# Kernel tuning notes

Measured on AMD Instinct MI355X. Metric: run time of the kernel, lower is better.

Reference implementation:

```python
import jax, jax.numpy as jnp
import numpy as np
from jax import lax

NUM_IM, ROIS = 32, 128          # images per batch, proposals per image
NUM_CLASSES, EMBED, OBJ_DIM = 151, 200, 2048
HALF_H = 256                    # per-direction LSTM hidden; bi concat -> 512
BN_EPS = 1e-5


def _lstm_dir(xs, wih, whh, b):
    # xs: [T, B, Din] -> hidden states [T, B, H]
    pre = jnp.einsum('tbd,dh->tbh', xs, wih) + b  # precompute input proj
    H = whh.shape[0]
    h0 = jnp.zeros((xs.shape[1], H), xs.dtype)
    def step(carry, pt):
        h, c = carry
        g = pt + h @ whh
        i, f, gg, o = jnp.split(g, 4, axis=-1)
        c = jax.nn.sigmoid(f) * c + jax.nn.sigmoid(i) * jnp.tanh(gg)
        h = jax.nn.sigmoid(o) * jnp.tanh(c)
        return (h, c), h
    _, hs = lax.scan(step, (h0, h0), pre)
    return hs


def _bilstm(x, wih, whh, b):
    # x: [B, T, D] -> [B, T, 2*HALF_H]; wih/whh/b carry both directions on axis 0
    xs = jnp.swapaxes(x, 0, 1)
    fwd = _lstm_dir(xs, wih[0], whh[0], b[0])
    bwd = _lstm_dir(xs[::-1], wih[1], whh[1], b[1])[::-1]
    return jnp.swapaxes(jnp.concatenate([fwd, bwd], -1), 0, 1)


def _context(feats, conf, params):
    # sort_rois: per-image descending confidence order, run 2-layer bi(tree)LSTM,
    # then scatter back with the inverse permutation (as in _sort_by_score).
    D = feats.shape[-1]
    f = feats.reshape(NUM_IM, ROIS, D)
    perm = jnp.argsort(-conf.reshape(NUM_IM, ROIS), axis=1)
    xs = jnp.take_along_axis(f, perm[..., None], axis=1)
    wih0, whh0, b0, wih1, whh1, b1 = params
    h = _bilstm(xs, wih0, whh0, b0)
    h = _bilstm(h, wih1, whh1, b1)
    inv = jnp.argsort(perm, axis=1)
    h = jnp.take_along_axis(h, inv[..., None], axis=1)
    return h.reshape(NUM_IM * ROIS, -1)


def setup_inputs() -> dict:
    key = jax.random.key(0)
    ks = jax.random.split(key, 24)
    N = NUM_IM * ROIS
    obj_fmaps = jax.random.normal(ks[0], (N, OBJ_DIM), jnp.float32)
    obj_logits = jax.random.normal(ks[1], (N, NUM_CLASSES), jnp.float32)
    xy = jax.random.uniform(ks[2], (N, 2), jnp.float32) * 500.0
    wh = jax.random.uniform(ks[3], (N, 2), jnp.float32) * 100.0 + 1.0
    boxes = jnp.concatenate([xy, xy + wh], axis=1)  # valid x1y1x2y2
    im_inds = jnp.repeat(jnp.arange(NUM_IM, dtype=jnp.int64), ROIS)
    w = lambda k, s: (jax.random.normal(k, s, jnp.float32) * 0.02)
    H4 = 4 * HALF_H
    D_obj, D_edge = OBJ_DIM + EMBED + 128, EMBED + 2 * HALF_H + OBJ_DIM
    return {
        'obj_fmaps': obj_fmaps, 'obj_logits': obj_logits, 'boxes': boxes,
        'im_inds': im_inds,
        'obj_embed_w': w(ks[4], (NUM_CLASSES, EMBED)),
        'obj_embed2_w': w(ks[5], (NUM_CLASSES, EMBED)),
        'bn_gamma': jnp.ones((4,), jnp.float32), 'bn_beta': jnp.zeros((4,), jnp.float32),
        'bn_mean': jnp.zeros((4,), jnp.float32), 'bn_var': jnp.ones((4,), jnp.float32),
        'pos_w': w(ks[6], (4, 128)), 'pos_b': jnp.zeros((128,), jnp.float32),
        'obj_wih0': w(ks[7], (2, D_obj, H4)), 'obj_whh0': w(ks[8], (2, HALF_H, H4)),
        'obj_b0': jnp.zeros((2, H4), jnp.float32),
        'obj_wih1': w(ks[9], (2, 2 * HALF_H, H4)), 'obj_whh1': w(ks[10], (2, HALF_H, H4)),
        'obj_b1': jnp.zeros((2, H4), jnp.float32),
        'edge_wih0': w(ks[11], (2, D_edge, H4)), 'edge_whh0': w(ks[12], (2, HALF_H, H4)),
        'edge_b0': jnp.zeros((2, H4), jnp.float32),
        'edge_wih1': w(ks[13], (2, 2 * HALF_H, H4)), 'edge_whh1': w(ks[14], (2, HALF_H, H4)),
        'edge_b1': jnp.zeros((2, H4), jnp.float32),
        'dec_w': w(ks[15], (D_obj + 2 * HALF_H, NUM_CLASSES)),
        'dec_b': jnp.zeros((NUM_CLASSES,), jnp.float32),
    }


def reference(obj_fmaps, obj_logits, boxes, im_inds, obj_embed_w, obj_embed2_w,
              bn_gamma, bn_beta, bn_mean, bn_var, pos_w, pos_b,
              obj_wih0, obj_whh0, obj_b0, obj_wih1, obj_whh1, obj_b1,
              edge_wih0, edge_whh0, edge_b0, edge_wih1, edge_whh1, edge_b1,
              dec_w, dec_b):
    probs = jax.nn.softmax(obj_logits, axis=-1)
    obj_embed = probs @ obj_embed_w                      # soft class embedding
    x1, y1, x2, y2 = boxes[:, 0], boxes[:, 1], boxes[:, 2], boxes[:, 3]
    cs = jnp.stack([(x1 + x2) * 0.5, (y1 + y2) * 0.5, x2 - x1, y2 - y1], axis=-1)
    csn = (cs - bn_mean) * lax.rsqrt(bn_var + BN_EPS) * bn_gamma + bn_beta
    pos = jax.nn.relu(csn @ pos_w + pos_b)               # BN(4)+Linear(4,128)+ReLU
    feats = jnp.concatenate([obj_fmaps, obj_embed, pos], axis=-1)  # [N, 2376]
    conf = jnp.max(probs[:, 1:], axis=-1)                # confidence (non-bg)
    enc = _context(feats, conf, (obj_wih0, obj_whh0, obj_b0,
                                 obj_wih1, obj_whh1, obj_b1))       # [N, 512]
    dec_in = jnp.concatenate([feats, enc], axis=-1)      # pass_in_obj_feats_to_decoder
    obj_dists = dec_in @ dec_w + dec_b                   # [N, 151]
    obj_preds = jnp.argmax(obj_dists[:, 1:], axis=-1) + 1
    edge_in = jnp.concatenate([obj_embed2_w[obj_preds], enc, obj_fmaps], axis=-1)
    edge_ctx = _context(edge_in, conf, (edge_wih0, edge_whh0, edge_b0,
                                        edge_wih1, edge_whh1, edge_b1))  # [N, 512]
    return jnp.concatenate([obj_dists, edge_ctx], axis=-1)  # [N, 663]
```

## Files before the change

kernel.cpp:

```cpp
#include <hip/hip_runtime.h>
#include <hip/hip_bf16.h>
#include <hip/hip_fp16.h>

typedef unsigned short u16;
typedef unsigned char u8;
typedef unsigned int u32;
typedef short s16x8 __attribute__((ext_vector_type(8)));
typedef float f32x4 __attribute__((ext_vector_type(4)));
typedef int i32x4 __attribute__((ext_vector_type(4)));

#define FE_LD 2944
#define EDGE_LD 2816

static __device__ __forceinline__ int sdot4(u32 a, u32 b, int acc) {
  return __builtin_amdgcn_sdot4((int)a, (int)b, acc, false);
}
static __device__ __forceinline__ float fsig(float x) {
  return __builtin_amdgcn_rcpf(1.f + __expf(-x));
}
static __device__ __forceinline__ float ftanh(float x) {
  return 1.f - 2.f * __builtin_amdgcn_rcpf(1.f + __expf(2.f * x));
}

#define GLD_LDS16(gsrc, ldst) \
  __builtin_amdgcn_global_load_lds((const __attribute__((address_space(1))) void*)(gsrc), \
                                   (__attribute__((address_space(3))) void*)(ldst), 16, 0, 0)

static __device__ __forceinline__ void xcd_map(int gy, int* bx, int* by) {
  int lin = blockIdx.x;
  int q = gridDim.x >> 3;
  int wg = (lin & 7) * q + (lin >> 3);
  *bx = wg / gy; *by = wg % gy;
}

__global__ __launch_bounds__(256) void gemm_kernel(
    const u16* __restrict__ A, int lda,
    const u16* __restrict__ B, int ldb,
    int K, int N, int gy,
    float* __restrict__ outF, __hip_bfloat16* __restrict__ outB, int ldc,
    const float* __restrict__ bias)
{
  __shared__ __align__(16) u16 As[128*64];
  __shared__ __align__(16) u16 Bs[128*64];
  const int tid = threadIdx.x;
  const int w = tid >> 6, lane = tid & 63;
  const int wm = w >> 1, wn = w & 1;
  int bxi, byi; xcd_map(gy, &bxi, &byi);
  const long bm = (long)bxi * 128;
  const long bn = (long)byi * 128;
  f32x4 acc[4][4] = {};

  for (int k0 = 0; k0 < K; k0 += 64) {
    #pragma unroll
    for (int rr = 0; rr < 4; rr++) {
      int idx = rr * 256 + tid;
      int row = idx >> 3;
      int g   = idx & 7;
      int gs  = g ^ (row & 7);
      int ldst = (rr * 256 + (w << 6)) * 8;
      GLD_LDS16(A + (bm + row) * (long)lda + k0 + gs * 8, &As[ldst]);
      GLD_LDS16(B + (bn + row) * (long)ldb + k0 + gs * 8, &Bs[ldst]);
    }
    __syncthreads();
    #pragma unroll
    for (int kk = 0; kk < 2; kk++) {
      s16x8 af[4], bfr[4];
      #pragma unroll
      for (int i = 0; i < 4; i++) {
        int ra = wm * 64 + i * 16 + (lane & 15);
        int rb = wn * 64 + i * 16 + (lane & 15);
        int gg = kk * 4 + (lane >> 4);
        af[i]  = *(const s16x8*)&As[ra * 64 + ((gg ^ (ra & 7)) << 3)];
        bfr[i] = *(const s16x8*)&Bs[rb * 64 + ((gg ^ (rb & 7)) << 3)];
      }
      #pragma unroll
      for (int i = 0; i < 4; i++)
        #pragma unroll
        for (int j = 0; j < 4; j++)
          acc[i][j] = __builtin_amdgcn_mfma_f32_16x16x32_bf16(af[i], bfr[j], acc[i][j], 0, 0, 0);
    }
    __syncthreads();
  }

  #pragma unroll
  for (int i = 0; i < 4; i++)
    #pragma unroll
    for (int j = 0; j < 4; j++)
      #pragma unroll
      for (int v = 0; v < 4; v++) {
        long rr = bm + wm * 64 + i * 16 + (lane >> 4) * 4 + v;
        int  cc = (int)bn + wn * 64 + j * 16 + (lane & 15);
        if (cc < N) {
          float val = acc[i][j][v] + (bias ? bias[cc] : 0.f);
          if (outF) outF[rr * (long)ldc + cc] = val;
          else      outB[rr * (long)ldc + cc] = __float2bfloat16(val);
        }
      }
}

__global__ __launch_bounds__(256) void gemm_i8_kernel(
    const u8* __restrict__ A, int lda,
    const u8* __restrict__ B, int ldb,
    int K, int N, int gy,
    const float* __restrict__ asc, const float* __restrict__ bsc,
    __hip_bfloat16* __restrict__ outB, int ldc,
    const float* __restrict__ bias)
{
  __shared__ __align__(16) u8 As[128*128];
  __shared__ __align__(16) u8 Bs[128*128];
  const int tid = threadIdx.x;
  const int w = tid >> 6, lane = tid & 63;
  const int wm = w >> 1, wn = w & 1;
  int bxi, byi; xcd_map(gy, &bxi, &byi);
  const long bm = (long)bxi * 128;
  const long bn = (long)byi * 128;
  i32x4 acc[4][4] = {};

  for (int k0 = 0; k0 < K; k0 += 128) {
    #pragma unroll
    for (int rr = 0; rr < 4; rr++) {
      int idx = rr * 256 + tid;
      int row = idx >> 3;
      int g   = idx & 7;
      int gs  = g ^ (row & 7);
      int ldst = (rr * 256 + (w << 6)) * 16;
      GLD_LDS16(A + (bm + row) * (long)lda + k0 + gs * 16, &As[ldst]);
      GLD_LDS16(B + (bn + row) * (long)ldb + k0 + gs * 16, &Bs[ldst]);
    }
    __syncthreads();
    #pragma unroll
    for (int kk = 0; kk < 2; kk++) {
      i32x4 af[4], bfr[4];
      #pragma unroll
      for (int i = 0; i < 4; i++) {
        int ra = wm * 64 + i * 16 + (lane & 15);
        int rb = wn * 64 + i * 16 + (lane & 15);
        int gg = kk * 4 + (lane >> 4);
        af[i]  = __builtin_bit_cast(i32x4, *(const uint4*)&As[ra * 128 + ((gg ^ (ra & 7)) << 4)]);
        bfr[i] = __builtin_bit_cast(i32x4, *(const uint4*)&Bs[rb * 128 + ((gg ^ (rb & 7)) << 4)]);
      }
      #pragma unroll
      for (int i = 0; i < 4; i++)
        #pragma unroll
        for (int j = 0; j < 4; j++)
          acc[i][j] = __builtin_amdgcn_mfma_i32_16x16x64_i8(af[i], bfr[j], acc[i][j], 0, 0, 0);
    }
    __syncthreads();
  }

  #pragma unroll
  for (int i = 0; i < 4; i++)
    #pragma unroll
    for (int j = 0; j < 4; j++)
      #pragma unroll
      for (int v = 0; v < 4; v++) {
        long rr = bm + wm * 64 + i * 16 + (lane >> 4) * 4 + v;
        int  cc = (int)bn + wn * 64 + j * 16 + (lane & 15);
        if (cc < N) {
          float val = (float)acc[i][j][v] * asc[rr] * bsc[cc] + (bias ? bias[cc] : 0.f);
          outB[rr * (long)ldc + cc] = __float2bfloat16(val);
        }
      }
}

__global__ void quant_rows(const u16* __restrict__ src, long ld, int K,
                           u8* __restrict__ dst, long dld, float* __restrict__ scale)
{
  __shared__ float red[256];
  const int row = blockIdx.x, t = threadIdx.x;
  const u16* s = src + (size_t)row * ld;
  float mx = 0.f;
  for (int c = t; c < K; c += 256) {
    u32 u = (u32)s[c] << 16;
    mx = fmaxf(mx, fabsf(__builtin_bit_cast(float, u)));
  }
  red[t] = mx; __syncthreads();
  for (int st = 128; st > 0; st >>= 1) { if (t < st) red[t] = fmaxf(red[t], red[t + st]); __syncthreads(); }
  mx = red[0];
  float inv = (mx > 0.f) ? 127.f / mx : 0.f;
  if (t == 0) scale[row] = (mx > 0.f) ? mx / 127.f : 0.f;
  u32* d32 = (u32*)(dst + (size_t)row * dld);
  for (int wd = t; wd < (K >> 2); wd += 256) {
    u32 v = 0;
    #pragma unroll
    for (int b = 0; b < 4; b++) {
      u32 u = (u32)s[4 * wd + b] << 16;
      int q = __float2int_rn(__builtin_bit_cast(float, u) * inv);
      q = max(-127, min(127, q));
      v |= ((u32)(q & 0xff)) << (8 * b);
    }
    d32[wd] = v;
  }
}

#define N_TROPS 10
struct TrOps {
  const float* src[N_TROPS];
  __hip_bfloat16* dst[N_TROPS];
  int srcK[N_TROPS], srcN[N_TROPS], dstR[N_TROPS], dstC[N_TROPS];
  int split[N_TROPS], soff[N_TROPS];
  int tileBase[N_TROPS], tilesX[N_TROPS];
};
__global__ void transpose_batch(TrOps ops)
{
  __shared__ float tile[32][33];
  int bid = blockIdx.x;
  int op = 0;
  #pragma unroll
  for (int i = 1; i < N_TROPS; i++) if (bid >= ops.tileBase[i]) op = i;
  const int local = bid - ops.tileBase[op];
  const int kt = (local % ops.tilesX[op]) * 32;
  const int nt = (local / ops.tilesX[op]) * 32;
  const float* src = ops.src[op];
  __hip_bfloat16* dst = ops.dst[op];
  const int srcK = ops.srcK[op], srcN = ops.srcN[op];
  const int dstR = ops.dstR[op], dstC = ops.dstC[op];
  const int split = ops.split[op], soff = ops.soff[op];

  const int tx = threadIdx.x & 31, ty = threadIdx.x >> 5;
  for (int i = ty; i < 32; i += 8) {
    int k = kt + i;
    int srck = (k < split) ? (soff + k) : (k - split);
    int n = nt + tx;
    tile[i][tx] = (srck < srcK && n < srcN) ? src[(size_t)srck * srcN + n] : 0.f;
  }
  __syncthreads();
  for (int i = ty; i < 32; i += 8) {
    int n = nt + i, k = kt + tx;
    if (n < dstR && k < dstC)
      dst[(size_t)n * dstC + k] = __float2bfloat16(tile[tx][i]);
  }
}

struct PkOps {
  const float* whh[4];
  u32* wreg[4];
  u32* wlds[4];
  float* wsc[4];
};
__global__ void pack_batch(PkOps ops)
{
  const int set = blockIdx.y;
  const float* whh = ops.whh[set];
  u32* wreg = ops.wreg[set];
  u32* wlds = ops.wlds[set];
  float* wsc = ops.wsc[set];

  const int idx = blockIdx.x * 256 + threadIdx.x;
  const int d = idx >> 10, col = idx & 1023;
  const int c4 = col >> 8, j = col & 255;
  const float* s = whh + (size_t)d * 256 * 1024 + col;
  float mx = 0.f;
  for (int k = 0; k < 256; k++) mx = fmaxf(mx, fabsf(s[(size_t)k * 1024]));
  float inv = (mx > 0.f) ? 127.f / mx : 0.f;
  wsc[d * 1024 + col] = (mx > 0.f) ? mx / (127.f * 127.f) : 0.f;
  const int rc = (c4 < 2) ? 12 : 8;
  const int rb = (c4 == 0) ? 0 : (c4 == 1) ? 12 : (c4 == 2) ? 24 : 32;
  for (int kg = 0; kg < 4; kg++) {
    const int slot = kg * 256 + j;
    for (int w = 0; w < 16; w++) {
      u32 v = 0;
      #pragma unroll
      for (int b = 0; b < 4; b++) {
        int q = __float2int_rn(s[(size_t)(kg * 64 + 4 * w + b) * 1024] * inv);
        q = max(-127, min(127, q));
        v |= ((u32)(q & 0xff)) << (8 * b);
      }
      if (w < rc) {
        wreg[(size_t)(d * 40 + rb + w) * 1024 + slot] = v;
      } else {
        int qq, comp;
        if (c4 == 0)      { qq = 0; comp = w - 12; }
        else if (c4 == 1) { qq = 1; comp = w - 12; }
        else if (c4 == 2) { qq = 2 + ((w - 8) >> 2); comp = (w - 8) & 3; }
        else              { qq = 4 + ((w - 8) >> 2); comp = (w - 8) & 3; }
        wlds[((size_t)(d * 6 + qq) * 1024 + slot) * 4 + comp] = v;
      }
    }
  }
}

__global__ void prep_kernel(
    const float* __restrict__ logits, const float* __restrict__ fmaps,
    const float* __restrict__ boxes,
    const float* __restrict__ bn_g, const float* __restrict__ bn_b,
    const float* __restrict__ bn_m, const float* __restrict__ bn_v,
    const float* __restrict__ pos_w, const float* __restrict__ pos_b,
    __hip_bfloat16* __restrict__ FE, __hip_bfloat16* __restrict__ probsb,
    float* __restrict__ conf)
{
  __shared__ float red[256];
  const int row = blockIdx.x, t = threadIdx.x;
  float v = (t < 151) ? logits[(size_t)row * 151 + t] : -3.0e38f;
  red[t] = v; __syncthreads();
  for (int s = 128; s > 0; s >>= 1) { if (t < s) red[t] = fmaxf(red[t], red[t + s]); __syncthreads(); }
  float mx = red[0]; __syncthreads();
  float p = (t < 151) ? expf(v - mx) : 0.f;
  red[t] = p; __syncthreads();
  for (int s = 128; s > 0; s >>= 1) { if (t < s) red[t] += red[t + s]; __syncthreads(); }
  float sum = red[0]; __syncthreads();
  p = p / sum;
  if (t < 192) probsb[(size_t)row * 192 + t] = __float2bfloat16((t < 151) ? p : 0.f);
  red[t] = (t >= 1 && t < 151) ? p : 0.f; __syncthreads();
  for (int s = 128; s > 0; s >>= 1) { if (t < s) red[t] = fmaxf(red[t], red[t + s]); __syncthreads(); }
  if (t == 0) conf[row] = red[0];

  if (t < 128) {
    float x1 = boxes[row * 4 + 0], y1 = boxes[row * 4 + 1];
    float x2 = boxes[row * 4 + 2], y2 = boxes[row * 4 + 3];
    float cs[4] = { (x1 + x2) * 0.5f, (y1 + y2) * 0.5f, x2 - x1, y2 - y1 };
    float a = pos_b[t];
    #pragma unroll
    for (int j = 0; j < 4; j++) {
      float cn = (cs[j] - bn_m[j]) * rsqrtf(bn_v[j] + 1e-5f) * bn_g[j] + bn_b[j];
      a += cn * pos_w[j * 128 + t];
    }
    FE[(size_t)row * FE_LD + 2760 + t] = __float2bfloat16(fmaxf(a, 0.f));
  }
  for (int c0 = t; c0 < 2048; c0 += 256)
    FE[(size_t)row * FE_LD + 512 + c0] = __float2bfloat16(fmaps[(size_t)row * 2048 + c0]);
}

__global__ void sort_kernel(const float* __restrict__ conf, int* __restrict__ perm)
{
  __shared__ float key[128];
  __shared__ int   idx[128];
  const int b = blockIdx.x, t = threadIdx.x;
  key[t] = conf[b * 128 + t]; idx[t] = t;
  __syncthreads();
  for (int k = 2; k <= 128; k <<= 1)
    for (int j = k >> 1; j > 0; j >>= 1) {
      int ixj = t ^ j;
      if (ixj > t) {
        bool up = (t & k) == 0;
        float ka = key[t], kb = key[ixj];
        int ia = idx[t], ib = idx[ixj];
        bool before = (ka > kb) || (ka == kb && ia < ib);
        if (before != up) { key[t] = kb; key[ixj] = ka; idx[t] = ib; idx[ixj] = ia; }
      }
      __syncthreads();
    }
  perm[b * 128 + t] = b * 128 + idx[t];
}

__global__ __launch_bounds__(1024) void rec_kernel(
    const __hip_bfloat16* __restrict__ P,
    const int* __restrict__ perm,
    const u32* __restrict__ wreg_g,
    const uint4* __restrict__ wlds_g,
    const float* __restrict__ wsc_g,
    int gatherPerm, int outPerm,
    __hip_bfloat16* __restrict__ out_bf, int out_ld,
    float* __restrict__ out_f32, int f32_ld, int f32_off)
{
  __shared__ __align__(16) uint4 wt4[6 * 1024];
  __shared__ __align__(16) int4 part[256 * 5];
  __shared__ __align__(16) u32 hq[64];
  __shared__ int prow_lds[128];
  const int tid = threadIdx.x;
  const int kg = tid >> 8;
  const int img = blockIdx.x & 31, dir = blockIdx.x >> 5;

  u32 wv[40];
  {
    const u32* rp = wreg_g + (size_t)dir * 40960 + tid;
    #pragma unroll
    for (int i = 0; i < 40; i++) wv[i] = rp[(size_t)i * 1024];
  }
  #pragma unroll
  for (int i = 0; i < 40; i++) asm volatile("" : "+v"(wv[i]));
  {
    const uint4* lp = wlds_g + (size_t)dir * 6144 + tid;
    #pragma unroll
    for (int q = 0; q < 6; q++) wt4[q * 1024 + tid] = lp[(size_t)q * 1024];
  }
  if (tid < 128) prow_lds[tid] = perm[img * 128 + tid];
  if (tid < 64) hq[tid] = 0;

  float sc0 = 0.f, sc1 = 0.f, sc2 = 0.f, sc3 = 0.f, cst = 0.f;
  if (tid < 256) {
    const float* sp = wsc_g + dir * 1024 + tid;
    sc0 = sp[0]; sc1 = sp[256]; sc2 = sp[512]; sc3 = sp[768];
  }
  __syncthreads();

  const uint4* hq4 = (const uint4*)hq;

  int st = dir ? 127 : 0;
  float p0 = 0.f, p1 = 0.f, p2 = 0.f, p3 = 0.f;
  if (tid < 256) {
    int prow0 = gatherPerm ? prow_lds[st] : (img * 128 + st);
    const __hip_bfloat16* pp = P + (size_t)prow0 * 2048 + dir * 1024 + tid;
    p0 = __bfloat162float(pp[0]);   p1 = __bfloat162float(pp[256]);
    p2 = __bfloat162float(pp[512]); p3 = __bfloat162float(pp[768]);
  }

  for (int t = 0; t < 128; t++) {
    float n0 = 0.f, n1 = 0.f, n2 = 0.f, n3 = 0.f;
    if (tid < 256 && t < 127) {
      int stn = dir ? (126 - t) : (t + 1);
      int prn = gatherPerm ? prow_lds[stn] : (img * 128 + stn);
      const __hip_bfloat16* pp = P + (size_t)prn * 2048 + dir * 1024 + tid;
      n0 = __bfloat162float(pp[0]);   n1 = __bfloat162float(pp[256]);
      n2 = __bfloat162float(pp[512]); n3 = __bfloat162float(pp[768]);
    }

    int a0 = 0, a1 = 0, a2 = 0, a3 = 0;
    {
      uint4 hv = hq4[kg * 4 + 0];
      a0 = sdot4(hv.x, wv[0], a0);  a0 = sdot4(hv.y, wv[1], a0);
      a0 = sdot4(hv.z, wv[2], a0);  a0 = sdot4(hv.w, wv[3], a0);
      a1 = sdot4(hv.x, wv[12], a1); a1 = sdot4(hv.y, wv[13], a1);
      a1 = sdot4(hv.z, wv[14], a1); a1 = sdot4(hv.w, wv[15], a1);
      a2 = sdot4(hv.x, wv[24], a2); a2 = sdot4(hv.y, wv[25], a2);
      a2 = sdot4(hv.z, wv[26], a2); a2 = sdot4(hv.w, wv[27], a2);
      a3 = sdot4(hv.x, wv[32], a3); a3 = sdot4(hv.y, wv[33], a3);
      a3 = sdot4(hv.z, wv[34], a3); a3 = sdot4(hv.w, wv[35], a3);
    }
    {
      uint4 hv = hq4[kg * 4 + 1];
      a0 = sdot4(hv.x, wv[4], a0);  a0 = sdot4(hv.y, wv[5], a0);
      a0 = sdot4(hv.z, wv[6], a0);  a0 = sdot4(hv.w, wv[7], a0);
      a1 = sdot4(hv.x, wv[16], a1); a1 = sdot4(hv.y, wv[17], a1);
      a1 = sdot4(hv.z, wv[18], a1); a1 = sdot4(hv.w, wv[19], a1);
      a2 = sdot4(hv.x, wv[28], a2); a2 = sdot4(hv.y, wv[29], a2);
      a2 = sdot4(hv.z, wv[30], a2); a2 = sdot4(hv.w, wv[31], a2);
      a3 = sdot4(hv.x, wv[36], a3); a3 = sdot4(hv.y, wv[37], a3);
      a3 = sdot4(hv.z, wv[38], a3); a3 = sdot4(hv.w, wv[39], a3);
    }
    {
      uint4 hv = hq4[kg * 4 + 2];
      a0 = sdot4(hv.x, wv[8], a0);  a0 = sdot4(hv.y, wv[9], a0);
      a0 = sdot4(hv.z, wv[10], a0); a0 = sdot4(hv.w, wv[11], a0);
      a1 = sdot4(hv.x, wv[20], a1); a1 = sdot4(hv.y, wv[21], a1);
      a1 = sdot4(hv.z, wv[22], a1); a1 = sdot4(hv.w, wv[23], a1);
      uint4 wl = wt4[2 * 1024 + tid];
      a2 = sdot4(hv.x, wl.x, a2); a2 = sdot4(hv.y, wl.y, a2);
      a2 = sdot4(hv.z, wl.z, a2); a2 = sdot4(hv.w, wl.w, a2);
      wl = wt4[4 * 1024 + tid];
      a3 = sdot4(hv.x, wl.x, a3); a3 = sdot4(hv.y, wl.y, a3);
      a3 = sdot4(hv.z, wl.z, a3); a3 = sdot4(hv.w, wl.w, a3);
    }
    {
      uint4 hv = hq4[kg * 4 + 3];
      uint4 wl = wt4[0 * 1024 + tid];
      a0 = sdot4(hv.x, wl.x, a0); a0 = sdot4(hv.y, wl.y, a0);
      a0 = sdot4(hv.z, wl.z, a0); a0 = sdot4(hv.w, wl.w, a0);
      wl = wt4[1 * 1024 + tid];
      a1 = sdot4(hv.x, wl.x, a1); a1 = sdot4(hv.y, wl.y, a1);
      a1 = sdot4(hv.z, wl.z, a1); a1 = sdot4(hv.w, wl.w, a1);
      wl = wt4[3 * 1024 + tid];
      a2 = sdot4(hv.x, wl.x, a2); a2 = sdot4(hv.y, wl.y, a2);
      a2 = sdot4(hv.z, wl.z, a2); a2 = sdot4(hv.w, wl.w, a2);
      wl = wt4[5 * 1024 + tid];
      a3 = sdot4(hv.x, wl.x, a3); a3 = sdot4(hv.y, wl.y, a3);
      a3 = sdot4(hv.z, wl.z, a3); a3 = sdot4(hv.w, wl.w, a3);
    }

    part[(tid & 255) * 5 + kg] = int4{a0, a1, a2, a3};
    __syncthreads();

    if (tid < 256) {
      int4 q0 = part[tid * 5 + 0], q1 = part[tid * 5 + 1];
      int4 q2 = part[tid * 5 + 2], q3 = part[tid * 5 + 3];
      float gi = (float)(q0.x + q1.x + q2.x + q3.x) * sc0 + p0;
      float gf = (float)(q0.y + q1.y + q2.y + q3.y) * sc1 + p1;
      float gg = (float)(q0.z + q1.z + q2.z + q3.z) * sc2 + p2;
      float go = (float)(q0.w + q1.w + q2.w + q3.w) * sc3 + p3;
      float si = fsig(gi), sf = fsig(gf), so = fsig(go);
      cst = sf * cst + si * ftanh(gg);
      float h = so * ftanh(cst);
      int qi = __float2int_rn(h * 127.f);
      ((signed char*)hq)[tid] = (signed char)qi;
      const int orow = outPerm ? prow_lds[st] : (img * 128 + st);
      if (out_bf)  out_bf[(size_t)orow * out_ld + dir * 256 + tid] = __float2bfloat16(h);
      if (out_f32) out_f32[(size_t)orow * f32_ld + f32_off + dir * 256 + tid] = h;
    }
    __syncthreads();
    p0 = n0; p1 = n1; p2 = n2; p3 = n3;
    st = dir ? (st - 1) : (st + 1);
  }
}

__global__ void argmax_edge_kernel(const float* __restrict__ dists,
                                   const float* __restrict__ embed2,
                                   const float* __restrict__ fmaps,
                                   const __hip_bfloat16* __restrict__ FE,
                                   __hip_bfloat16* __restrict__ EDGE)
{
  __shared__ float rv[256];
  __shared__ int   ri[256];
  const int row = blockIdx.x, t = threadIdx.x;

  float best = (t < 150) ? dists[(size_t)row * 663 + 1 + t] : -3.4e38f;
  int   bi   = (t < 150) ? (1 + t) : 1000;
  rv[t] = best; ri[t] = bi;
  __syncthreads();
  for (int s = 128; s > 0; s >>= 1) {
    if (t < s) {
      float ov = rv[t + s]; int oi = ri[t + s];
      if (ov > rv[t] || (ov == rv[t] && oi < ri[t])) { rv[t] = ov; ri[t] = oi; }
    }
    __syncthreads();
  }
  const int pr = ri[0];

  for (int c0 = t; c0 < 200; c0 += 256)
    EDGE[(size_t)row * EDGE_LD + c0] = __float2bfloat16(embed2[(size_t)pr * 200 + c0]);
  for (int c0 = t; c0 < 512; c0 += 256)
    EDGE[(size_t)row * EDGE_LD + 200 + c0] = FE[(size_t)row * FE_LD + c0];
  for (int c0 = t; c0 < 2048; c0 += 256)
    EDGE[(size_t)row * EDGE_LD + 712 + c0] = __float2bfloat16(fmaps[(size_t)row * 2048 + c0]);
}

extern "C" void kernel_launch(void* const* d_in, const int* in_sizes, int n_in,
                              void* d_out, int out_size, void* d_ws, size_t ws_size,
                              hipStream_t stream)
{
  const float* obj_fmaps    = (const float*)d_in[0];
  const float* obj_logits   = (const float*)d_in[1];
  const float* boxes        = (const float*)d_in[2];
  const float* obj_embed_w  = (const float*)d_in[4];
  const float* obj_embed2_w = (const float*)d_in[5];
  const float* bn_g = (const float*)d_in[6];
  const float* bn_b = (const float*)d_in[7];
  const float* bn_m = (const float*)d_in[8];
  const float* bn_v = (const float*)d_in[9];
  const float* pos_w = (const float*)d_in[10];
  const float* pos_b = (const float*)d_in[11];
  const float* obj_wih0 = (const float*)d_in[12];
  const float* obj_whh0 = (const float*)d_in[13];
  const float* obj_b0   = (const float*)d_in[14];
  const float* obj_wih1 = (const float*)d_in[15];
  const float* obj_whh1 = (const float*)d_in[16];
  const float* obj_b1   = (const float*)d_in[17];
  const float* edge_wih0 = (const float*)d_in[18];
  const float* edge_whh0 = (const float*)d_in[19];
  const float* edge_b0   = (const float*)d_in[20];
  const float* edge_wih1 = (const float*)d_in[21];
  const float* edge_whh1 = (const float*)d_in[22];
  const float* edge_b1   = (const float*)d_in[23];
  const float* dec_w = (const float*)d_in[24];
  const float* dec_b = (const float*)d_in[25];
  float* out = (float*)d_out;

  char* ws = (char*)d_ws;
  auto alloc = [&](size_t bytes) -> char* {
    char* p = ws; ws += (bytes + 255) & ~(size_t)255; return p;
  };
  __hip_bfloat16* FE     = (__hip_bfloat16*)alloc(4096ull * FE_LD * 2);
  __hip_bfloat16* EDGE   = (__hip_bfloat16*)alloc(4096ull * EDGE_LD * 2);
  __hip_bfloat16* Pbuf   = (__hip_bfloat16*)alloc(4096ull * 2048 * 2);
  __hip_bfloat16* hseq   = (__hip_bfloat16*)alloc(4096ull * 512 * 2);
  __hip_bfloat16* probsb = (__hip_bfloat16*)alloc(4096ull * 192 * 2);
  __hip_bfloat16* wih0T  = (__hip_bfloat16*)alloc(2048ull * 2432 * 2);
  __hip_bfloat16* wih1T  = (__hip_bfloat16*)alloc(2048ull * 512 * 2);
  __hip_bfloat16* ewih0T = (__hip_bfloat16*)alloc(2048ull * 2816 * 2);
  __hip_bfloat16* ewih1T = (__hip_bfloat16*)alloc(2048ull * 512 * 2);
  __hip_bfloat16* embedT = (__hip_bfloat16*)alloc(256ull * 192 * 2);
  __hip_bfloat16* decT   = (__hip_bfloat16*)alloc(256ull * 2944 * 2);
  u32* whh0pk  = (u32*)alloc(133120ull * 4);
  u32* whh1pk  = (u32*)alloc(133120ull * 4);
  u32* ewhh0pk = (u32*)alloc(133120ull * 4);
  u32* ewhh1pk = (u32*)alloc(133120ull * 4);
  u8*  FEq     = (u8*)alloc(4096ull * 2432);
  u8*  EDGEq   = (u8*)alloc(4096ull * 2816);
  u8*  wih0q   = (u8*)alloc(2048ull * 2432);
  u8*  ewih0q  = (u8*)alloc(2048ull * 2816);
  float* ascFE   = (float*)alloc(4096 * 4);
  float* ascEDGE = (float*)alloc(4096 * 4);
  float* bsc0    = (float*)alloc(2048 * 4);
  float* bsc1    = (float*)alloc(2048 * 4);
  int*   perm  = (int*)alloc(4096 * 4);
  float* conf  = (float*)alloc(4096 * 4);
  (void)in_sizes; (void)n_in; (void)out_size; (void)ws_size;

  TrOps tr{};
  int nt = 0, base = 0;
  auto addTr = [&](const float* src, __hip_bfloat16* dst, int srcK, int srcN,
                   int dstR, int dstC, int split, int soff) {
    tr.src[nt] = src; tr.dst[nt] = dst;
    tr.srcK[nt] = srcK; tr.srcN[nt] = srcN; tr.dstR[nt] = dstR; tr.dstC[nt] = dstC;
    tr.split[nt] = split; tr.soff[nt] = soff;
    int tx = (dstC + 31) / 32, ty = (dstR + 31) / 32;
    tr.tileBase[nt] = base; tr.tilesX[nt] = tx;
    base += tx * ty; nt++;
  };
  for (int d = 0; d < 2; d++) {
    addTr(obj_wih0 + (size_t)d * 2376 * 1024, wih0T + (size_t)d * 1024 * 2432, 2376, 1024, 1024, 2432, 0, 0);
    addTr(obj_wih1 + (size_t)d * 512 * 1024,  wih1T + (size_t)d * 1024 * 512,  512, 1024, 1024, 512, 0, 0);
    addTr(edge_wih0 + (size_t)d * 2760 * 1024, ewih0T + (size_t)d * 1024 * 2816, 2760, 1024, 1024, 2816, 0, 0);
    addTr(edge_wih1 + (size_t)d * 512 * 1024,  ewih1T + (size_t)d * 1024 * 512,  512, 1024, 1024, 512, 0, 0);
  }
  addTr(obj_embed_w, embedT, 151, 200, 256, 192, 0, 0);
  addTr(dec_w, decT, 2888, 151, 256, 2944, 512, 2376);
  transpose_batch<<<dim3(base), dim3(256), 0, stream>>>(tr);

  PkOps pk{};
  const float* whhs[4] = {obj_whh0, obj_whh1, edge_whh0, edge_whh1};
  u32* pks[4] = {whh0pk, whh1pk, ewhh0pk, ewhh1pk};
  for (int i = 0; i < 4; i++) {
    pk.whh[i] = whhs[i];
    pk.wreg[i] = pks[i];
    pk.wlds[i] = pks[i] + 81920;
    pk.wsc[i]  = (float*)(pks[i] + 131072);
  }
  pack_batch<<<dim3(8, 4), dim3(256), 0, stream>>>(pk);

  quant_rows<<<dim3(2048), dim3(256), 0, stream>>>((const u16*)wih0T, 2432, 2432, wih0q, 2432, bsc0);
  quant_rows<<<dim3(2048), dim3(256), 0, stream>>>((const u16*)ewih0T, 2816, 2816, ewih0q, 2816, bsc1);

  prep_kernel<<<dim3(4096), dim3(256), 0, stream>>>(
      obj_logits, obj_fmaps, boxes, bn_g, bn_b, bn_m, bn_v, pos_w, pos_b, FE, probsb, conf);
  sort_kernel<<<dim3(32), dim3(128), 0, stream>>>(conf, perm);

  auto gemm = [&](const void* A, int lda, const void* B, int ldb, int K, int N,
                  float* oF, __hip_bfloat16* oB, int ldc, const float* bias) {
    int gy = (N + 127) / 128;
    gemm_kernel<<<dim3(32 * gy), dim3(256), 0, stream>>>(
        (const u16*)A, lda, (const u16*)B, ldb, K, N, gy, oF, oB, ldc, bias);
  };
  auto gemm_i8 = [&](const u8* A, int lda, const u8* B, int ldb, int K, int N,
                     const float* asc, const float* bsc,
                     __hip_bfloat16* oB, int ldc, const float* bias) {
    int gy = (N + 127) / 128;
    gemm_i8_kernel<<<dim3(32 * gy), dim3(256), 0, stream>>>(
        A, lda, B, ldb, K, N, gy, asc, bsc, oB, ldc, bias);
  };
  auto rec = [&](const __hip_bfloat16* P, const u32* wpk, int gat, int op,
                 __hip_bfloat16* ob, int old_, float* of, int fld, int foff) {
    rec_kernel<<<dim3(64), dim3(1024), 0, stream>>>(
        P, perm, wpk, (const uint4*)(wpk + 81920), (const float*)(wpk + 131072),
        gat, op, ob, old_, of, fld, foff);
  };

  gemm(probsb, 192, embedT, 192, 192, 200, nullptr, FE + 2560, FE_LD, nullptr);
  quant_rows<<<dim3(4096), dim3(256), 0, stream>>>((const u16*)FE + 512, FE_LD, 2432, FEq, 2432, ascFE);
  gemm_i8(FEq, 2432, wih0q, 2432, 2432, 2048, ascFE, bsc0, Pbuf, 2048, obj_b0);
  rec(Pbuf, whh0pk, 1, 0, hseq, 512, nullptr, 0, 0);
  gemm(hseq, 512, wih1T, 512, 512, 2048, nullptr, Pbuf, 2048, obj_b1);
  rec(Pbuf, whh1pk, 0, 1, FE, FE_LD, nullptr, 0, 0);
  gemm(FE, FE_LD, decT, 2944, 2944, 151, out, nullptr, 663, dec_b);
  argmax_edge_kernel<<<dim3(4096), dim3(256), 0, stream>>>(
      out, obj_embed2_w, obj_fmaps, FE, EDGE);
  quant_rows<<<dim3(4096), dim3(256), 0, stream>>>((const u16*)EDGE, EDGE_LD, 2816, EDGEq, 2816, ascEDGE);
  gemm_i8(EDGEq, 2816, ewih0q, 2816, 2816, 2048, ascEDGE, bsc1, Pbuf, 2048, edge_b0);
  rec(Pbuf, ewhh0pk, 1, 0, hseq, 512, nullptr, 0, 0);
  gemm(hseq, 512, ewih1T, 512, 512, 2048, nullptr, Pbuf, 2048, edge_b1);
  rec(Pbuf, ewhh1pk, 0, 1, nullptr, 0, out, 663, 151);
}
```

Baseline: 864.2 us.

## Fuse setup kernels and activation quantization into producer kernels

Merges the transpose, pack and prep kernels into one setup kernel, and the weight-quant and sort kernels into another, to cut launch count. The soft-embedding GEMM now runs inline in the prep path, and the FE row is quantized to int8 directly from an fp32 LDS stage. The EDGE activation buffer is dropped because argmax_edge now quantizes its row straight to int8. The costs are a per-row 151x200 scalar dot loop, heavier LDS use per block, and quantization from fp32 values where it used to read bf16-rounded ones, which can change the int8 results slightly.

Result: faster. 822.4 us (-4.8%).

```diff
diff --git a/kernel.cpp b/kernel.cpp
--- a/kernel.cpp
+++ b/kernel.cpp
@@ -163,135 +163,101 @@
       }
 }
 
-__global__ void quant_rows(const u16* __restrict__ src, long ld, int K,
-                           u8* __restrict__ dst, long dld, float* __restrict__ scale)
-{
-  __shared__ float red[256];
-  const int row = blockIdx.x, t = threadIdx.x;
-  const u16* s = src + (size_t)row * ld;
-  float mx = 0.f;
-  for (int c = t; c < K; c += 256) {
-    u32 u = (u32)s[c] << 16;
-    mx = fmaxf(mx, fabsf(__builtin_bit_cast(float, u)));
-  }
-  red[t] = mx; __syncthreads();
-  for (int st = 128; st > 0; st >>= 1) { if (t < st) red[t] = fmaxf(red[t], red[t + st]); __syncthreads(); }
-  mx = red[0];
-  float inv = (mx > 0.f) ? 127.f / mx : 0.f;
-  if (t == 0) scale[row] = (mx > 0.f) ? mx / 127.f : 0.f;
-  u32* d32 = (u32*)(dst + (size_t)row * dld);
-  for (int wd = t; wd < (K >> 2); wd += 256) {
-    u32 v = 0;
-    #pragma unroll
-    for (int b = 0; b < 4; b++) {
-      u32 u = (u32)s[4 * wd + b] << 16;
-      int q = __float2int_rn(__builtin_bit_cast(float, u) * inv);
-      q = max(-127, min(127, q));
-      v |= ((u32)(q & 0xff)) << (8 * b);
-    }
-    d32[wd] = v;
-  }
-}
-
-#define N_TROPS 10
-struct TrOps {
+#define N_TROPS 9
+struct SetupOps {
   const float* src[N_TROPS];
   __hip_bfloat16* dst[N_TROPS];
   int srcK[N_TROPS], srcN[N_TROPS], dstR[N_TROPS], dstC[N_TROPS];
   int split[N_TROPS], soff[N_TROPS];
   int tileBase[N_TROPS], tilesX[N_TROPS];
+  int trEnd, pkEnd;
+  const float* whh[4];
+  u32* wreg[4]; u32* wlds[4]; float* wsc[4];
+  const float* logits; const float* fmaps; const float* boxes;
+  const float* bn_g; const float* bn_b; const float* bn_m; const float* bn_v;
+  const float* pos_w; const float* pos_b; const float* embw;
+  __hip_bfloat16* FE; u8* FEq; float* ascFE; float* conf;
 };
-__global__ void transpose_batch(TrOps ops)
+__global__ __launch_bounds__(256) void setup_kernel(SetupOps ops)
 {
-  __shared__ float tile[32][33];
-  int bid = blockIdx.x;
-  int op = 0;
-  #pragma unroll
-  for (int i = 1; i < N_TROPS; i++) if (bid >= ops.tileBase[i]) op = i;
-  const int local = bid - ops.tileBase[op];
-  const int kt = (local % ops.tilesX[op]) * 32;
-  const int nt = (local / ops.tilesX[op]) * 32;
-  const float* src = ops.src[op];
-  __hip_bfloat16* dst = ops.dst[op];
-  const int srcK = ops.srcK[op], srcN = ops.srcN[op];
-  const int dstR = ops.dstR[op], dstC = ops.dstC[op];
-  const int split = ops.split[op], soff = ops.soff[op];
-
-  const int tx = threadIdx.x & 31, ty = threadIdx.x >> 5;
-  for (int i = ty; i < 32; i += 8) {
-    int k = kt + i;
-    int srck = (k < split) ? (soff + k) : (k - split);
-    int n = nt + tx;
-    tile[i][tx] = (srck < srcK && n < srcN) ? src[(size_t)srck * srcN + n] : 0.f;
-  }
-  __syncthreads();
-  for (int i = ty; i < 32; i += 8) {
-    int n = nt + i, k = kt + tx;
-    if (n < dstR && k < dstC)
-      dst[(size_t)n * dstC + k] = __float2bfloat16(tile[tx][i]);
-  }
-}
-
-struct PkOps {
-  const float* whh[4];
-  u32* wreg[4];
-  u32* wlds[4];
-  float* wsc[4];
-};
-__global__ void pack_batch(PkOps ops)
-{
-  const int set = blockIdx.y;
-  const float* whh = ops.whh[set];
-  u32* wreg = ops.wreg[set];
-  u32* wlds = ops.wlds[set];
-  float* wsc = ops.wsc[set];
-
-  const int idx = blockIdx.x * 256 + threadIdx.x;
-  const int d = idx >> 10, col = idx & 1023;
-  const int c4 = col >> 8, j = col & 255;
-  const float* s = whh + (size_t)d * 256 * 1024 + col;
-  float mx = 0.f;
-  for (int k = 0; k < 256; k++) mx = fmaxf(mx, fabsf(s[(size_t)k * 1024]));
-  float inv = (mx > 0.f) ? 127.f / mx : 0.f;
-  wsc[d * 1024 + col] = (mx > 0.f) ? mx / (127.f * 127.f) : 0.f;
-  const int rc = (c4 < 2) ? 12 : 8;
-  const int rb = (c4 == 0) ? 0 : (c4 == 1) ? 12 : (c4 == 2) ? 24 : 32;
-  for (int kg = 0; kg < 4; kg++) {
-    const int slot = kg * 256 + j;
-    for (int w = 0; w < 16; w++) {
-      u32 v = 0;
-      #pragma unroll
-      for (int b = 0; b < 4; b++) {
-        int q = __float2int_rn(s[(size_t)(kg * 64 + 4 * w + b) * 1024] * inv);
-        q = max(-127, min(127, q));
-        v |= ((u32)(q & 0xff)) << (8 * b);
+  __shared__ float stage[2432];
+  __shared__ float red[256];
+  __shared__ float pf[151];
+  const int bid = blockIdx.x, t = threadIdx.x;
+
+  if (bid < ops.trEnd) {
+    __shared__ float tile[32][33];
+    int op = 0;
+    #pragma unroll
+    for (int i = 1; i < N_TROPS; i++) if (bid >= ops.tileBase[i]) op = i;
+    const int local = bid - ops.tileBase[op];
+    const int kt = (local % ops.tilesX[op]) * 32;
+    const int nt = (local / ops.tilesX[op]) * 32;
+    const float* src = ops.src[op];
+    __hip_bfloat16* dst = ops.dst[op];
+    const int srcK = ops.srcK[op], srcN = ops.srcN[op];
+    const int dstR = ops.dstR[op], dstC = ops.dstC[op];
+    const int split = ops.split[op], soff = ops.soff[op];
+    const int tx = t & 31, ty = t >> 5;
+    for (int i = ty; i < 32; i += 8) {
+      int k = kt + i;
+      int srck = (k < split) ? (soff + k) : (k - split);
+      int n = nt + tx;
+      tile[i][tx] = (srck < srcK && n < srcN) ? src[(size_t)srck * srcN + n] : 0.f;
+    }
+    __syncthreads();
+    for (int i = ty; i < 32; i += 8) {
+      int n = nt + i, k = kt + tx;
+      if (n < dstR && k < dstC)
+        dst[(size_t)n * dstC + k] = __float2bfloat16(tile[tx][i]);
+    }
+    return;
+  }
+
+  if (bid < ops.pkEnd) {
+    const int local = bid - ops.trEnd;
+    const int set = local >> 3;
+    const int idx = (local & 7) * 256 + t;
+    const float* whh = ops.whh[set];
+    u32* wreg = ops.wreg[set];
+    u32* wlds = ops.wlds[set];
+    float* wsc = ops.wsc[set];
+    const int d = idx >> 10, col = idx & 1023;
+    const int c4 = col >> 8, j = col & 255;
+    const float* s = whh + (size_t)d * 256 * 1024 + col;
+    float mx = 0.f;
+    for (int k = 0; k < 256; k++) mx = fmaxf(mx, fabsf(s[(size_t)k * 1024]));
+    float inv = (mx > 0.f) ? 127.f / mx : 0.f;
+    wsc[d * 1024 + col] = (mx > 0.f) ? mx / (127.f * 127.f) : 0.f;
+    const int rc = (c4 < 2) ? 12 : 8;
+    const int rb = (c4 == 0) ? 0 : (c4 == 1) ? 12 : (c4 == 2) ? 24 : 32;
+    for (int kg = 0; kg < 4; kg++) {
+      const int slot = kg * 256 + j;
+      for (int w = 0; w < 16; w++) {
+        u32 v = 0;
+        #pragma unroll
+        for (int b = 0; b < 4; b++) {
+          int q = __float2int_rn(s[(size_t)(kg * 64 + 4 * w + b) * 1024] * inv);
+          q = max(-127, min(127, q));
+          v |= ((u32)(q & 0xff)) << (8 * b);
+        }
+        if (w < rc) {
+          wreg[(size_t)(d * 40 + rb + w) * 1024 + slot] = v;
+        } else {
+          int qq, comp;
+          if (c4 == 0)      { qq = 0; comp = w - 12; }
+          else if (c4 == 1) { qq = 1; comp = w - 12; }
+          else if (c4 == 2) { qq = 2 + ((w - 8) >> 2); comp = (w - 8) & 3; }
+          else              { qq = 4 + ((w - 8) >> 2); comp = (w - 8) & 3; }
+          wlds[((size_t)(d * 6 + qq) * 1024 + slot) * 4 + comp] = v;
+        }
       }
-      if (w < rc) {
-        wreg[(size_t)(d * 40 + rb + w) * 1024 + slot] = v;
-      } else {
-        int qq, comp;
-        if (c4 == 0)      { qq = 0; comp = w - 12; }
-        else if (c4 == 1) { qq = 1; comp = w - 12; }
-        else if (c4 == 2) { qq = 2 + ((w - 8) >> 2); comp = (w - 8) & 3; }
-        else              { qq = 4 + ((w - 8) >> 2); comp = (w - 8) & 3; }
-        wlds[((size_t)(d * 6 + qq) * 1024 + slot) * 4 + comp] = v;
-      }
-    }
-  }
-}
-
-__global__ void prep_kernel(
-    const float* __restrict__ logits, const float* __restrict__ fmaps,
-    const float* __restrict__ boxes,
-    const float* __restrict__ bn_g, const float* __restrict__ bn_b,
-    const float* __restrict__ bn_m, const float* __restrict__ bn_v,
-    const float* __restrict__ pos_w, const float* __restrict__ pos_b,
-    __hip_bfloat16* __restrict__ FE, __hip_bfloat16* __restrict__ probsb,
-    float* __restrict__ conf)
-{
-  __shared__ float red[256];
-  const int row = blockIdx.x, t = threadIdx.x;
-  float v = (t < 151) ? logits[(size_t)row * 151 + t] : -3.0e38f;
+    }
+    return;
+  }
+
+  const int row = bid - ops.pkEnd;
+  float v = (t < 151) ? ops.logits[(size_t)row * 151 + t] : -3.0e38f;
   red[t] = v; __syncthreads();
   for (int s = 128; s > 0; s >>= 1) { if (t < s) red[t] = fmaxf(red[t], red[t + s]); __syncthreads(); }
   float mx = red[0]; __syncthreads();
@@ -300,47 +266,121 @@
   for (int s = 128; s > 0; s >>= 1) { if (t < s) red[t] += red[t + s]; __syncthreads(); }
   float sum = red[0]; __syncthreads();
   p = p / sum;
-  if (t < 192) probsb[(size_t)row * 192 + t] = __float2bfloat16((t < 151) ? p : 0.f);
+  if (t < 151) pf[t] = p;
   red[t] = (t >= 1 && t < 151) ? p : 0.f; __syncthreads();
   for (int s = 128; s > 0; s >>= 1) { if (t < s) red[t] = fmaxf(red[t], red[t + s]); __syncthreads(); }
-  if (t == 0) conf[row] = red[0];
-
+  if (t == 0) ops.conf[row] = red[0];
+  __syncthreads();
+
+  __hip_bfloat16* FE = ops.FE + (size_t)row * FE_LD;
+  for (int c0 = t; c0 < 2048; c0 += 256) {
+    float f = ops.fmaps[(size_t)row * 2048 + c0];
+    stage[c0] = f;
+    FE[512 + c0] = __float2bfloat16(f);
+  }
+  for (int c = t; c < 200; c += 256) {
+    float e = 0.f;
+    for (int k = 0; k < 151; k++) e += pf[k] * ops.embw[(size_t)k * 200 + c];
+    stage[2048 + c] = e;
+    FE[2560 + c] = __float2bfloat16(e);
+  }
   if (t < 128) {
-    float x1 = boxes[row * 4 + 0], y1 = boxes[row * 4 + 1];
-    float x2 = boxes[row * 4 + 2], y2 = boxes[row * 4 + 3];
+    float x1 = ops.boxes[row * 4 + 0], y1 = ops.boxes[row * 4 + 1];
+    float x2 = ops.boxes[row * 4 + 2], y2 = ops.boxes[row * 4 + 3];
     float cs[4] = { (x1 + x2) * 0.5f, (y1 + y2) * 0.5f, x2 - x1, y2 - y1 };
-    float a = pos_b[t];
+    float a = ops.pos_b[t];
     #pragma unroll
     for (int j = 0; j < 4; j++) {
-      float cn = (cs[j] - bn_m[j]) * rsqrtf(bn_v[j] + 1e-5f) * bn_g[j] + bn_b[j];
-      a += cn * pos_w[j * 128 + t];
-    }
-    FE[(size_t)row * FE_LD + 2760 + t] = __float2bfloat16(fmaxf(a, 0.f));
-  }
-  for (int c0 = t; c0 < 2048; c0 += 256)
-    FE[(size_t)row * FE_LD + 512 + c0] = __float2bfloat16(fmaps[(size_t)row * 2048 + c0]);
-}
-
-__global__ void sort_kernel(const float* __restrict__ conf, int* __restrict__ perm)
+      float cn = (cs[j] - ops.bn_m[j]) * rsqrtf(ops.bn_v[j] + 1e-5f) * ops.bn_g[j] + ops.bn_b[j];
+      a += cn * ops.pos_w[j * 128 + t];
+    }
+    a = fmaxf(a, 0.f);
+    stage[2248 + t] = a;
+    FE[2760 + t] = __float2bfloat16(a);
+  }
+  if (t < 56) { stage[2376 + t] = 0.f; FE[2888 + t] = __float2bfloat16(0.f); }
+  __syncthreads();
+
+  float qm = 0.f;
+  for (int c = t; c < 2432; c += 256) qm = fmaxf(qm, fabsf(stage[c]));
+  red[t] = qm; __syncthreads();
+  for (int s = 128; s > 0; s >>= 1) { if (t < s) red[t] = fmaxf(red[t], red[t + s]); __syncthreads(); }
+  qm = red[0];
+  float inv = (qm > 0.f) ? 127.f / qm : 0.f;
+  if (t == 0) ops.ascFE[row] = (qm > 0.f) ? qm / 127.f : 0.f;
+  u32* d32 = (u32*)(ops.FEq + (size_t)row * 2432);
+  for (int wd = t; wd < 608; wd += 256) {
+    u32 vv = 0;
+    #pragma unroll
+    for (int b = 0; b < 4; b++) {
+      int q = __float2int_rn(stage[4 * wd + b] * inv);
+      q = max(-127, min(127, q));
+      vv |= ((u32)(q & 0xff)) << (8 * b);
+    }
+    d32[wd] = vv;
+  }
+}
+
+__global__ __launch_bounds__(256) void quantw_sort_kernel(
+    const u16* __restrict__ w0, u8* __restrict__ w0q, float* __restrict__ bsc0,
+    const u16* __restrict__ w1, u8* __restrict__ w1q, float* __restrict__ bsc1,
+    const float* __restrict__ conf, int* __restrict__ perm)
 {
-  __shared__ float key[128];
-  __shared__ int   idx[128];
-  const int b = blockIdx.x, t = threadIdx.x;
-  key[t] = conf[b * 128 + t]; idx[t] = t;
-  __syncthreads();
-  for (int k = 2; k <= 128; k <<= 1)
-    for (int j = k >> 1; j > 0; j >>= 1) {
-      int ixj = t ^ j;
-      if (ixj > t) {
-        bool up = (t & k) == 0;
-        float ka = key[t], kb = key[ixj];
-        int ia = idx[t], ib = idx[ixj];
-        bool before = (ka > kb) || (ka == kb && ia < ib);
-        if (before != up) { key[t] = kb; key[ixj] = ka; idx[t] = ib; idx[ixj] = ia; }
+  const int bid = blockIdx.x, t = threadIdx.x;
+  if (bid < 4096) {
+    __shared__ float red[256];
+    const int row = (bid < 2048) ? bid : (bid - 2048);
+    const u16* src = (bid < 2048) ? w0 : w1;
+    u8* dst = (bid < 2048) ? w0q : w1q;
+    float* sc = (bid < 2048) ? bsc0 : bsc1;
+    const int K = (bid < 2048) ? 2432 : 2816;
+    const u16* s = src + (size_t)row * K;
+    float mx = 0.f;
+    for (int c = t; c < K; c += 256) {
+      u32 u = (u32)s[c] << 16;
+      mx = fmaxf(mx, fabsf(__builtin_bit_cast(float, u)));
+    }
+    red[t] = mx; __syncthreads();
+    for (int st = 128; st > 0; st >>= 1) { if (t < st) red[t] = fmaxf(red[t], red[t + st]); __syncthreads(); }
+    mx = red[0];
+    float inv = (mx > 0.f) ? 127.f / mx : 0.f;
+    if (t == 0) sc[row] = (mx > 0.f) ? mx / 127.f : 0.f;
+    u32* d32 = (u32*)(dst + (size_t)row * K);
+    for (int wd = t; wd < (K >> 2); wd += 256) {
+      u32 v = 0;
+      #pragma unroll
+      for (int b = 0; b < 4; b++) {
+        u32 u = (u32)s[4 * wd + b] << 16;
+        int q = __float2int_rn(__builtin_bit_cast(float, u) * inv);
+        q = max(-127, min(127, q));
+        v |= ((u32)(q & 0xff)) << (8 * b);
       }
-      __syncthreads();
-    }
-  perm[b * 128 + t] = b * 128 + idx[t];
+      d32[wd] = v;
+    }
+    return;
+  }
+  {
+    __shared__ float key[128];
+    __shared__ int   idx[128];
+    const int b = bid - 4096;
+    if (t < 128) { key[t] = conf[b * 128 + t]; idx[t] = t; }
+    __syncthreads();
+    for (int k = 2; k <= 128; k <<= 1)
+      for (int j = k >> 1; j > 0; j >>= 1) {
+        if (t < 128) {
+          int ixj = t ^ j;
+          if (ixj > t) {
+            bool up = (t & k) == 0;
+            float ka = key[t], kb = key[ixj];
+            int ia = idx[t], ib = idx[ixj];
+            bool before = (ka > kb) || (ka == kb && ia < ib);
+            if (before != up) { key[t] = kb; key[ixj] = ka; idx[t] = ib; idx[ixj] = ia; }
+          }
+        }
+        __syncthreads();
+      }
+    if (t < 128) perm[b * 128 + t] = b * 128 + idx[t];
+  }
 }
 
 __global__ __launch_bounds__(1024) void rec_kernel(
@@ -482,12 +522,14 @@
   }
 }
 
-__global__ void argmax_edge_kernel(const float* __restrict__ dists,
-                                   const float* __restrict__ embed2,
-                                   const float* __restrict__ fmaps,
-                                   const __hip_bfloat16* __restrict__ FE,
-                                   __hip_bfloat16* __restrict__ EDGE)
+__global__ __launch_bounds__(256) void argmax_edge_kernel(
+    const float* __restrict__ dists,
+    const float* __restrict__ embed2,
+    const float* __restrict__ fmaps,
+    const __hip_bfloat16* __restrict__ FE,
+    u8* __restrict__ EDGEq, float* __restrict__ ascEDGE)
 {
+  __shared__ float stage[EDGE_LD];
   __shared__ float rv[256];
   __shared__ int   ri[256];
   const int row = blockIdx.x, t = threadIdx.x;
@@ -506,11 +548,32 @@
   const int pr = ri[0];
 
   for (int c0 = t; c0 < 200; c0 += 256)
-    EDGE[(size_t)row * EDGE_LD + c0] = __float2bfloat16(embed2[(size_t)pr * 200 + c0]);
+    stage[c0] = embed2[(size_t)pr * 200 + c0];
   for (int c0 = t; c0 < 512; c0 += 256)
-    EDGE[(size_t)row * EDGE_LD + 200 + c0] = FE[(size_t)row * FE_LD + c0];
+    stage[200 + c0] = __bfloat162float(FE[(size_t)row * FE_LD + c0]);
   for (int c0 = t; c0 < 2048; c0 += 256)
-    EDGE[(size_t)row * EDGE_LD + 712 + c0] = __float2bfloat16(fmaps[(size_t)row * 2048 + c0]);
+    stage[712 + c0] = fmaps[(size_t)row * 2048 + c0];
+  if (t < 56) stage[2760 + t] = 0.f;
+  __syncthreads();
+
+  float qm = 0.f;
+  for (int c = t; c < EDGE_LD; c += 256) qm = fmaxf(qm, fabsf(stage[c]));
+  rv[t] = qm; __syncthreads();
+  for (int s = 128; s > 0; s >>= 1) { if (t < s) rv[t] = fmaxf(rv[t], rv[t + s]); __syncthreads(); }
+  qm = rv[0];
+  float inv = (qm > 0.f) ? 127.f / qm : 0.f;
+  if (t == 0) ascEDGE[row] = (qm > 0.f) ? qm / 127.f : 0.f;
+  u32* d32 = (u32*)(EDGEq + (size_t)row * EDGE_LD);
+  for (int wd = t; wd < (EDGE_LD >> 2); wd += 256) {
+    u32 vv = 0;
+    #pragma unroll
+    for (int b = 0; b < 4; b++) {
+      int q = __float2int_rn(stage[4 * wd + b] * inv);
+      q = max(-127, min(127, q));
+      vv |= ((u32)(q & 0xff)) << (8 * b);
+    }
+    d32[wd] = vv;
+  }
 }
 
 extern "C" void kernel_launch(void* const* d_in, const int* in_sizes, int n_in,
@@ -549,15 +612,12 @@
     char* p = ws; ws += (bytes + 255) & ~(size_t)255; return p;
   };
   __hip_bfloat16* FE     = (__hip_bfloat16*)alloc(4096ull * FE_LD * 2);
-  __hip_bfloat16* EDGE   = (__hip_bfloat16*)alloc(4096ull * EDGE_LD * 2);
   __hip_bfloat16* Pbuf   = (__hip_bfloat16*)alloc(4096ull * 2048 * 2);
   __hip_bfloat16* hseq   = (__hip_bfloat16*)alloc(4096ull * 512 * 2);
-  __hip_bfloat16* probsb = (__hip_bfloat16*)alloc(4096ull * 192 * 2);
   __hip_bfloat16* wih0T  = (__hip_bfloat16*)alloc(2048ull * 2432 * 2);
   __hip_bfloat16* wih1T  = (__hip_bfloat16*)alloc(2048ull * 512 * 2);
   __hip_bfloat16* ewih0T = (__hip_bfloat16*)alloc(2048ull * 2816 * 2);
   __hip_bfloat16* ewih1T = (__hip_bfloat16*)alloc(2048ull * 512 * 2);
-  __hip_bfloat16* embedT = (__hip_bfloat16*)alloc(256ull * 192 * 2);
   __hip_bfloat16* decT   = (__hip_bfloat16*)alloc(256ull * 2944 * 2);
   u32* whh0pk  = (u32*)alloc(133120ull * 4);
   u32* whh1pk  = (u32*)alloc(133120ull * 4);
@@ -575,15 +635,15 @@
   float* conf  = (float*)alloc(4096 * 4);
   (void)in_sizes; (void)n_in; (void)out_size; (void)ws_size;
 
-  TrOps tr{};
+  SetupOps so{};
   int nt = 0, base = 0;
   auto addTr = [&](const float* src, __hip_bfloat16* dst, int srcK, int srcN,
                    int dstR, int dstC, int split, int soff) {
-    tr.src[nt] = src; tr.dst[nt] = dst;
-    tr.srcK[nt] = srcK; tr.srcN[nt] = srcN; tr.dstR[nt] = dstR; tr.dstC[nt] = dstC;
-    tr.split[nt] = split; tr.soff[nt] = soff;
+    so.src[nt] = src; so.dst[nt] = dst;
+    so.srcK[nt] = srcK; so.srcN[nt] = srcN; so.dstR[nt] = dstR; so.dstC[nt] = dstC;
+    so.split[nt] = split; so.soff[nt] = soff;
     int tx = (dstC + 31) / 32, ty = (dstR + 31) / 32;
-    tr.tileBase[nt] = base; tr.tilesX[nt] = tx;
+    so.tileBase[nt] = base; so.tilesX[nt] = tx;
     base += tx * ty; nt++;
   };
   for (int d = 0; d < 2; d++) {
@@ -592,27 +652,25 @@
     addTr(edge_wih0 + (size_t)d * 2760 * 1024, ewih0T + (size_t)d * 1024 * 2816, 2760, 1024, 1024, 2816, 0, 0);
     addTr(edge_wih1 + (size_t)d * 512 * 1024,  ewih1T + (size_t)d * 1024 * 512,  512, 1024, 1024, 512, 0, 0);
   }
-  addTr(obj_embed_w, embedT, 151, 200, 256, 192, 0, 0);
   addTr(dec_w, decT, 2888, 151, 256, 2944, 512, 2376);
-  transpose_batch<<<dim3(base), dim3(256), 0, stream>>>(tr);
-
-  PkOps pk{};
+  so.trEnd = base;
+  so.pkEnd = base + 32;
   const float* whhs[4] = {obj_whh0, obj_whh1, edge_whh0, edge_whh1};
   u32* pks[4] = {whh0pk, whh1pk, ewhh0pk, ewhh1pk};
   for (int i = 0; i < 4; i++) {
-    pk.whh[i] = whhs[i];
-    pk.wreg[i] = pks[i];
-    pk.wlds[i] = pks[i] + 81920;
-    pk.wsc[i]  = (float*)(pks[i] + 131072);
-  }
-  pack_batch<<<dim3(8, 4), dim3(256), 0, stream>>>(pk);
-
-  quant_rows<<<dim3(2048), dim3(256), 0, stream>>>((const u16*)wih0T, 2432, 2432, wih0q, 2432, bsc0);
-  quant_rows<<<dim3(2048), dim3(256), 0, stream>>>((const u16*)ewih0T, 2816, 2816, ewih0q, 2816, bsc1);
-
-  prep_kernel<<<dim3(4096), dim3(256), 0, stream>>>(
-      obj_logits, obj_fmaps, boxes, bn_g, bn_b, bn_m, bn_v, pos_w, pos_b, FE, probsb, conf);
-  sort_kernel<<<dim3(32), dim3(128), 0, stream>>>(conf, perm);
+    so.whh[i] = whhs[i];
+    so.wreg[i] = pks[i];
+    so.wlds[i] = pks[i] + 81920;
+    so.wsc[i]  = (float*)(pks[i] + 131072);
+  }
+  so.logits = obj_logits; so.fmaps = obj_fmaps; so.boxes = boxes;
+  so.bn_g = bn_g; so.bn_b = bn_b; so.bn_m = bn_m; so.bn_v = bn_v;
+  so.pos_w = pos_w; so.pos_b = pos_b; so.embw = obj_embed_w;
+  so.FE = FE; so.FEq = FEq; so.ascFE = ascFE; so.conf = conf;
+  setup_kernel<<<dim3(so.pkEnd + 4096), dim3(256), 0, stream>>>(so);
+
+  quantw_sort_kernel<<<dim3(4128), dim3(256), 0, stream>>>(
+      (const u16*)wih0T, wih0q, bsc0, (const u16*)ewih0T, ewih0q, bsc1, conf, perm);
 
   auto gemm = [&](const void* A, int lda, const void* B, int ldb, int K, int N,
                   float* oF, __hip_bfloat16* oB, int ldc, const float* bias) {
@@ -634,16 +692,13 @@
         gat, op, ob, old_, of, fld, foff);
   };
 
-  gemm(probsb, 192, embedT, 192, 192, 200, nullptr, FE + 2560, FE_LD, nullptr);
-  quant_rows<<<dim3(4096), dim3(256), 0, stream>>>((const u16*)FE + 512, FE_LD, 2432, FEq, 2432, ascFE);
   gemm_i8(FEq, 2432, wih0q, 2432, 2432, 2048, ascFE, bsc0, Pbuf, 2048, obj_b0);
   rec(Pbuf, whh0pk, 1, 0, hseq, 512, nullptr, 0, 0);
   gemm(hseq, 512, wih1T, 512, 512, 2048, nullptr, Pbuf, 2048, obj_b1);
   rec(Pbuf, whh1pk, 0, 1, FE, FE_LD, nullptr, 0, 0);
   gemm(FE, FE_LD, decT, 2944, 2944, 151, out, nullptr, 663, dec_b);
   argmax_edge_kernel<<<dim3(4096), dim3(256), 0, stream>>>(
-      out, obj_embed2_w, obj_fmaps, FE, EDGE);
-  quant_rows<<<dim3(4096), dim3(256), 0, stream>>>((const u16*)EDGE, EDGE_LD, 2816, EDGEq, 2816, ascEDGE);
+      out, obj_embed2_w, obj_fmaps, FE, EDGEq, ascEDGE);
   gemm_i8(EDGEq, 2816, ewih0q, 2816, 2816, 2048, ascEDGE, bsc1, Pbuf, 2048, edge_b0);
   rec(Pbuf, ewhh0pk, 1, 0, hseq, 512, nullptr, 0, 0);
   gemm(hseq, 512, ewih1T, 512, 512, 2048, nullptr, Pbuf, 2048, edge_b1);
```
